# Performance work log

Hardware: AMD Instinct MI355X
Metric: run time of the kernel (lower is better)

The kernel has to match this reference:

```python
import jax, jax.numpy as jnp
import numpy as np

B, U, L, E, H, V = 512, 10, 50, 200, 200, 50000
FLAT = 16 * 16 * 8  # conv(3x3,VALID)->48x48, pool(3x3,s3)->16x16, 8 channels


def gru(x, Wih, Whh, bih, bhh):
    """PyTorch-convention GRU (gate order r,z,n). x: [B,T,E] -> (ys [B,T,H], h_last [B,H])."""
    Bx = x.shape[0]
    Hh = Whh.shape[1]
    x_proj = x @ Wih.T + bih  # [B,T,3H]

    def step(h, xp):
        gh = h @ Whh.T + bhh
        xr, xz, xn = jnp.split(xp, 3, axis=-1)
        hr, hz, hn = jnp.split(gh, 3, axis=-1)
        r = jax.nn.sigmoid(xr + hr)
        z = jax.nn.sigmoid(xz + hz)
        n = jnp.tanh(xn + r * hn)
        h_new = (1.0 - z) * n + z * h
        return h_new, h_new

    h0 = jnp.zeros((Bx, Hh), x.dtype)
    h_last, ys = jax.lax.scan(step, h0, jnp.swapaxes(x_proj, 0, 1))
    return jnp.swapaxes(ys, 0, 1), h_last


def setup_inputs() -> dict:
    key = jax.random.key(0)
    ks = jax.random.split(key, 24)
    s = 0.05
    inp = {
        "utterance": jax.random.randint(ks[0], (B, U, L), 0, V, dtype=jnp.int32),
        "response": jax.random.randint(ks[1], (B, L), 0, V, dtype=jnp.int32),
        "emb": jax.random.uniform(ks[2], (V, E), jnp.float32, -0.25, 0.25),
        "W_ih_u": jax.random.normal(ks[3], (3 * H, E)) * s,
        "W_hh_u": jax.random.normal(ks[4], (3 * H, H)) * s,
        "b_ih_u": jnp.zeros((3 * H,), jnp.float32),
        "b_hh_u": jnp.zeros((3 * H,), jnp.float32),
        "W_ih_r": jax.random.normal(ks[5], (3 * H, E)) * s,
        "W_hh_r": jax.random.normal(ks[6], (3 * H, H)) * s,
        "b_ih_r": jnp.zeros((3 * H,), jnp.float32),
        "b_hh_r": jnp.zeros((3 * H,), jnp.float32),
        "conv_w": jax.random.normal(ks[7], (8, 2, 3, 3)) * 0.3,
        "conv_b": jnp.zeros((8,), jnp.float32),
        "lin_w": jax.random.normal(ks[8], (50, FLAT)) * 0.02,
        "lin_b": jnp.zeros((50,), jnp.float32),
        "Amat": jax.random.normal(ks[9], (H, H)) * 0.05,
        "W_ih_f": jax.random.normal(ks[10], (3 * H, 50)) * s,
        "W_hh_f": jax.random.normal(ks[11], (3 * H, H)) * s,
        "b_ih_f": jnp.zeros((3 * H,), jnp.float32),
        "b_hh_f": jnp.zeros((3 * H,), jnp.float32),
        "flin_w": jax.random.normal(ks[12], (1, H)) * 0.05,
        "flin_b": jnp.zeros((1,), jnp.float32),
    }
    return inp


def reference(utterance, response, emb, W_ih_u, W_hh_u, b_ih_u, b_hh_u,
              W_ih_r, W_hh_r, b_ih_r, b_hh_r, conv_w, conv_b, lin_w, lin_b,
              Amat, W_ih_f, W_hh_f, b_ih_f, b_hh_f, flin_w, flin_b):
    ue = emb[utterance]            # [B,U,L,E]
    re = emb[response]             # [B,L,E]

    rg, _ = gru(re, W_ih_r, W_hh_r, b_ih_r, b_hh_r)  # [B,L,H]

    # word-level match: matmul(utt_emb, resp_emb^T)
    m1 = jnp.einsum('bule,bte->bult', ue, re)  # [B,U,L,L]

    # segment-level: GRU(utt) @ A @ GRU(resp)^T  (loop over utterances folded into batch)
    ug, _ = gru(ue.reshape(B * U, L, E), W_ih_u, W_hh_u, b_ih_u, b_hh_u)
    ug = ug.reshape(B, U, L, H)
    m2 = jnp.einsum('bulh,hk,btk->bult', ug, Amat, rg)  # [B,U,L,L]

    x = jnp.stack([m1, m2], axis=2).reshape(B * U, 2, L, L)  # [B*U,2,50,50]
    x = jax.lax.conv_general_dilated(x, conv_w, (1, 1), 'VALID',
                                     dimension_numbers=('NCHW', 'OIHW', 'NCHW'))
    x = jax.nn.relu(x + conv_b[None, :, None, None])          # [B*U,8,48,48]
    x = jax.lax.reduce_window(x, -jnp.inf, jax.lax.max,
                              (1, 1, 3, 3), (1, 1, 3, 3), 'VALID')  # [B*U,8,16,16]
    x = x.reshape(B * U, FLAT)
    mv = jnp.tanh(x @ lin_w.T + lin_b).reshape(B, U, 50)      # matching vectors

    _, h_last = gru(mv, W_ih_f, W_hh_f, b_ih_f, b_hh_f)       # [B,H]
    logits = h_last @ flin_w.T + flin_b                       # [B,1]
    return jax.nn.sigmoid(logits)
```

## Files before the change

### kernel.cpp

```cpp
#include <hip/hip_runtime.h>
#include <hip/hip_bf16.h>


typedef __attribute__((ext_vector_type(8))) short short8v;
typedef __attribute__((ext_vector_type(4))) float f32x4;

__device__ __forceinline__ float sigm(float x) { return 1.0f / (1.0f + __expf(-x)); }
__device__ __forceinline__ float tanhfast(float x) {
    float e = __expf(2.0f * x);
    return 1.0f - 2.0f / (e + 1.0f);
}
__device__ __forceinline__ float bl(unsigned x) { return __uint_as_float(x << 16); }
__device__ __forceinline__ float bh(unsigned x) { return __uint_as_float(x & 0xffff0000u); }
__device__ __forceinline__ unsigned packbf(float a, float b) {
    union { __hip_bfloat16 h[2]; unsigned u; } cv;
    cv.h[0] = __float2bfloat16(a); cv.h[1] = __float2bfloat16(b);
    return cv.u;
}

__global__ __launch_bounds__(256)
void gemm_mfma(const void* __restrict__ Asrc, int a_bf16,
               const int* __restrict__ gidx,
               const float* __restrict__ W, const float* __restrict__ bias,
               __hip_bfloat16* __restrict__ C, int M, int N)
{
    __shared__ __hip_bfloat16 Al[64 * 232];
    __shared__ __hip_bfloat16 Bl[64 * 232];
    const int tid = threadIdx.x;
    const int m0 = blockIdx.x * 64, n0 = blockIdx.y * 64;

    for (int idx = tid; idx < 64 * 29; idx += 256) {
        int r = idx / 29, q = idx - r * 29;
        int k0 = q * 8, row = m0 + r;
        uint4 val = make_uint4(0, 0, 0, 0);
        if (k0 < 200 && row < M) {
            size_t ar = (size_t)(gidx ? gidx[row] : row) * 200 + k0;
            if (a_bf16) {
                val = *(const uint4*)((const __hip_bfloat16*)Asrc + ar);
            } else {
                const float* ap = (const float*)Asrc + ar;
                float4 f0 = *(const float4*)ap;
                float4 f1 = *(const float4*)(ap + 4);
                val.x = packbf(f0.x, f0.y); val.y = packbf(f0.z, f0.w);
                val.z = packbf(f1.x, f1.y); val.w = packbf(f1.z, f1.w);
            }
        }
        *(uint4*)(Al + r * 232 + k0) = val;
    }
    for (int idx = tid; idx < 64 * 29; idx += 256) {
        int r = idx / 29, q = idx - r * 29;
        int k0 = q * 8, row = n0 + r;
        uint4 val = make_uint4(0, 0, 0, 0);
        if (k0 < 200 && row < N) {
            const float* wp = W + (size_t)row * 200 + k0;
            float4 f0 = *(const float4*)wp;
            float4 f1 = *(const float4*)(wp + 4);
            val.x = packbf(f0.x, f0.y); val.y = packbf(f0.z, f0.w);
            val.z = packbf(f1.x, f1.y); val.w = packbf(f1.z, f1.w);
        }
        *(uint4*)(Bl + r * 232 + k0) = val;
    }
    __syncthreads();

    const int wid = tid >> 6, lane = tid & 63;
    const int wm = (wid >> 1) * 32, wn = (wid & 1) * 32;
    const int lrow = lane & 15, lk8 = (lane >> 4) * 8;
    f32x4 acc00 = {0.f, 0.f, 0.f, 0.f}, acc01 = {0.f, 0.f, 0.f, 0.f};
    f32x4 acc10 = {0.f, 0.f, 0.f, 0.f}, acc11 = {0.f, 0.f, 0.f, 0.f};
#pragma unroll
    for (int kk = 0; kk < 7; ++kk) {
        const int kb = kk * 32 + lk8;
        short8v a0 = *(const short8v*)(Al + (wm + lrow) * 232 + kb);
        short8v a1 = *(const short8v*)(Al + (wm + 16 + lrow) * 232 + kb);
        short8v b0 = *(const short8v*)(Bl + (wn + lrow) * 232 + kb);
        short8v b1 = *(const short8v*)(Bl + (wn + 16 + lrow) * 232 + kb);
        acc00 = __builtin_amdgcn_mfma_f32_16x16x32_bf16(a0, b0, acc00, 0, 0, 0);
        acc01 = __builtin_amdgcn_mfma_f32_16x16x32_bf16(a0, b1, acc01, 0, 0, 0);
        acc10 = __builtin_amdgcn_mfma_f32_16x16x32_bf16(a1, b0, acc10, 0, 0, 0);
        acc11 = __builtin_amdgcn_mfma_f32_16x16x32_bf16(a1, b1, acc11, 0, 0, 0);
    }
    const int drow = (lane >> 4) * 4, dcol = lane & 15;
#pragma unroll
    for (int fm = 0; fm < 2; ++fm) {
#pragma unroll
        for (int fn = 0; fn < 2; ++fn) {
            const f32x4 av = (fm == 0) ? (fn == 0 ? acc00 : acc01)
                                       : (fn == 0 ? acc10 : acc11);
            const int gcol = n0 + wn + fn * 16 + dcol;
            if (gcol >= N) continue;
            const float bs = bias ? bias[gcol] : 0.0f;
#pragma unroll
            for (int r = 0; r < 4; ++r) {
                const int grow = m0 + wm + fm * 16 + drow + r;
                if (grow >= M) continue;
                C[(size_t)grow * N + gcol] = __float2bfloat16(av[r] + bs);
            }
        }
    }
}

__global__ __launch_bounds__(256)
void gemm_tn(const void* __restrict__ Av, int a_bf16,
             const int* __restrict__ gidx, int gstride, int goff,
             const float* __restrict__ W, const float* __restrict__ bias,
             void* __restrict__ Cv, int c_bf16,
             int M, int N, int K, int act)
{
    __shared__ float As[16][64];
    __shared__ float Ws[16][64];
    const int tid = threadIdx.x;
    const int m0 = blockIdx.x * 64;
    const int n0 = blockIdx.y * 64;
    const int lr = tid >> 2;
    const int lk = (tid & 3) << 2;
    const int tx = tid & 15, ty = tid >> 4;

    float acc[4][4];
#pragma unroll
    for (int i = 0; i < 4; ++i)
#pragma unroll
        for (int j = 0; j < 4; ++j) acc[i][j] = 0.0f;

    const int am = m0 + lr;
    size_t arow_off = 0; bool avalid = (am < M);
    if (avalid) arow_off = (size_t)(gidx ? gidx[(size_t)am * gstride + goff] : am) * K;
    const float* arow32 = (const float*)Av + arow_off;
    const __hip_bfloat16* arow16 = (const __hip_bfloat16*)Av + arow_off;
    const int wn = n0 + lr;
    const float* wrow = (wn < N) ? (W + (size_t)wn * K) : nullptr;

    for (int kb = 0; kb < K; kb += 16) {
        const int k = kb + lk;
        float a0 = 0, a1 = 0, a2 = 0, a3 = 0, w0 = 0, w1 = 0, w2 = 0, w3 = 0;
        if (avalid) {
            if (a_bf16) {
                if (k + 3 < K) {
                    uint2 p = *(const uint2*)(arow16 + k);
                    a0 = bl(p.x); a1 = bh(p.x); a2 = bl(p.y); a3 = bh(p.y);
                } else {
                    if (k < K) a0 = __bfloat162float(arow16[k]);
                    if (k + 1 < K) a1 = __bfloat162float(arow16[k + 1]);
                    if (k + 2 < K) a2 = __bfloat162float(arow16[k + 2]);
                }
            } else {
                if (k + 3 < K) { float4 v = *(const float4*)(arow32 + k); a0 = v.x; a1 = v.y; a2 = v.z; a3 = v.w; }
                else { if (k < K) a0 = arow32[k]; if (k + 1 < K) a1 = arow32[k + 1]; if (k + 2 < K) a2 = arow32[k + 2]; }
            }
        }
        if (wrow) {
            if (k + 3 < K) { float4 v = *(const float4*)(wrow + k); w0 = v.x; w1 = v.y; w2 = v.z; w3 = v.w; }
            else { if (k < K) w0 = wrow[k]; if (k + 1 < K) w1 = wrow[k + 1]; if (k + 2 < K) w2 = wrow[k + 2]; }
        }
        __syncthreads();
        As[lk + 0][lr] = a0; As[lk + 1][lr] = a1; As[lk + 2][lr] = a2; As[lk + 3][lr] = a3;
        Ws[lk + 0][lr] = w0; Ws[lk + 1][lr] = w1; Ws[lk + 2][lr] = w2; Ws[lk + 3][lr] = w3;
        __syncthreads();
#pragma unroll
        for (int kk = 0; kk < 16; ++kk) {
            float4 av = *(const float4*)(&As[kk][ty << 2]);
            float4 wv = *(const float4*)(&Ws[kk][tx << 2]);
            float aa[4] = { av.x, av.y, av.z, av.w };
            float ww[4] = { wv.x, wv.y, wv.z, wv.w };
#pragma unroll
            for (int i = 0; i < 4; ++i)
#pragma unroll
                for (int j = 0; j < 4; ++j)
                    acc[i][j] = fmaf(aa[i], ww[j], acc[i][j]);
        }
    }

#pragma unroll
    for (int i = 0; i < 4; ++i) {
        const int row = m0 + (ty << 2) + i;
        if (row >= M) continue;
#pragma unroll
        for (int j = 0; j < 4; ++j) {
            const int col = n0 + (tx << 2) + j;
            if (col >= N) continue;
            float t = acc[i][j];
            if (bias) t += bias[col];
            if (act == 1) t = tanhfast(t);
            if (c_bf16) ((__hip_bfloat16*)Cv)[(size_t)row * N + col] = __float2bfloat16(t);
            else        ((float*)Cv)[(size_t)row * N + col] = t;
        }
    }
}

__global__ __launch_bounds__(256)
void transpose_wf(const float* __restrict__ Wf, float* __restrict__ Tf)
{
    int id = blockIdx.x * 256 + threadIdx.x;
    if (id < 120000) {
        int e = id / 600, j = id - e * 600;
        Tf[id] = Wf[(size_t)j * 200 + e];
    }
}

__global__ __launch_bounds__(256)
void pack_whh(const float* __restrict__ Wu, const float* __restrict__ Wr,
              __hip_bfloat16* __restrict__ Du, __hip_bfloat16* __restrict__ Dr)
{
    int idx = blockIdx.x * 256 + threadIdx.x;
    if (idx >= 136192) return;
    int j = idx / 224, e = idx - j * 224;
    bool v = (j < 600) && (e < 200);
    Du[idx] = __float2bfloat16(v ? Wu[(size_t)j * 200 + e] : 0.0f);
    Dr[idx] = __float2bfloat16(v ? Wr[(size_t)j * 200 + e] : 0.0f);
}

__global__ __launch_bounds__(256)
void gather_re16(const int* __restrict__ resp, const float* __restrict__ emb,
                 __hip_bfloat16* __restrict__ re16)
{
    int idx = blockIdx.x * 256 + threadIdx.x;
    if (idx < 2560000) {
        int row = idx / 100, q = idx - row * 100;
        float2 v = *(const float2*)(emb + (size_t)resp[row] * 200 + 2 * q);
        ((unsigned*)re16)[idx] = packbf(v.x, v.y);
    }
}

__global__ __launch_bounds__(512)
void scan_gru_mfma(const int* __restrict__ utt,
                   const __hip_bfloat16* __restrict__ EPu,
                   const __hip_bfloat16* __restrict__ xpr16,
                   const __hip_bfloat16* __restrict__ Wu16,
                   const __hip_bfloat16* __restrict__ Wr16,
                   const float* __restrict__ bhu, const float* __restrict__ bhr,
                   __hip_bfloat16* __restrict__ ug16,
                   __hip_bfloat16* __restrict__ rg16)
{
    __shared__ __align__(16) float gh[32][612];
    __shared__ __align__(16) float hf[32][204];
    __shared__ __align__(16) __hip_bfloat16 h16[32][232];

    const int tid = threadIdx.x;
    const bool isResp = (int)blockIdx.x >= 160;
    const int row0 = isResp ? ((int)blockIdx.x - 160) * 32 : (int)blockIdx.x * 32;
    const __hip_bfloat16* Wt = isResp ? Wr16 : Wu16;
    const float* bgate = isResp ? bhr : bhu;
    __hip_bfloat16* arch = isResp ? rg16 : ug16;

    for (int i = tid; i < 32 * 204; i += 512) ((float*)hf)[i] = 0.0f;
    for (int i = tid; i < 928; i += 512) ((uint4*)h16)[i] = make_uint4(0, 0, 0, 0);
    __syncthreads();

    const int wid = tid >> 6, lane = tid & 63;
    const int ntBase = (wid < 6) ? wid * 5 : 30 + (wid - 6) * 4;
    const int ntCnt  = (wid < 6) ? 5 : 4;
    const int lrow = lane & 15, lk8 = (lane >> 4) * 8;
    const int drow = (lane >> 4) * 4, dcol = lane & 15;

    for (int t = 0; t < 50; ++t) {
        f32x4 a0[5], a1[5];
#pragma unroll
        for (int i = 0; i < 5; ++i) {
            a0[i] = (f32x4){0.f, 0.f, 0.f, 0.f};
            a1[i] = (f32x4){0.f, 0.f, 0.f, 0.f};
        }
#pragma unroll
        for (int kk = 0; kk < 7; ++kk) {
            short8v A0 = *(const short8v*)(&h16[lrow][kk * 32 + lk8]);
            short8v A1 = *(const short8v*)(&h16[16 + lrow][kk * 32 + lk8]);
#pragma unroll
            for (int i = 0; i < 5; ++i) {
                if (i < ntCnt) {
                    const int j = (ntBase + i) * 16 + lrow;
                    short8v B = *(const short8v*)(Wt + (size_t)j * 224 + kk * 32 + lk8);
                    a0[i] = __builtin_amdgcn_mfma_f32_16x16x32_bf16(A0, B, a0[i], 0, 0, 0);
                    a1[i] = __builtin_amdgcn_mfma_f32_16x16x32_bf16(A1, B, a1[i], 0, 0, 0);
                }
            }
        }
#pragma unroll
        for (int i = 0; i < 5; ++i) {
            if (i < ntCnt) {
                const int j = (ntBase + i) * 16 + dcol;
#pragma unroll
                for (int r = 0; r < 4; ++r) {
                    gh[drow + r][j] = a0[i][r];
                    gh[16 + drow + r][j] = a1[i][r];
                }
            }
        }
        __syncthreads();
        for (int task = tid; task < 800; task += 512) {
            const int row = task / 25;
            const int c0 = (task - row * 25) * 8;
            const int grow = row0 + row;
            const __hip_bfloat16* xp = isResp
                ? (xpr16 + ((size_t)grow * 50 + t) * 600)
                : (EPu + (size_t)utt[grow * 50 + t] * 600);
            uint4 xrv = *(const uint4*)(xp + c0);
            uint4 xzv = *(const uint4*)(xp + 200 + c0);
            uint4 xnv = *(const uint4*)(xp + 400 + c0);
            const unsigned xra[4] = { xrv.x, xrv.y, xrv.z, xrv.w };
            const unsigned xza[4] = { xzv.x, xzv.y, xzv.z, xzv.w };
            const unsigned xna[4] = { xnv.x, xnv.y, xnv.z, xnv.w };
            float hn[8];
#pragma unroll
            for (int j = 0; j < 8; ++j) {
                const int c = c0 + j;
                const float xr = (j & 1) ? bh(xra[j >> 1]) : bl(xra[j >> 1]);
                const float xz = (j & 1) ? bh(xza[j >> 1]) : bl(xza[j >> 1]);
                const float xn = (j & 1) ? bh(xna[j >> 1]) : bl(xna[j >> 1]);
                const float rr = sigm(xr + gh[row][c] + bgate[c]);
                const float zz = sigm(xz + gh[row][200 + c] + bgate[200 + c]);
                const float nn = tanhfast(xn + rr * (gh[row][400 + c] + bgate[400 + c]));
                hn[j] = (1.0f - zz) * nn + zz * hf[row][c];
            }
            *(float4*)(&hf[row][c0])     = (float4){hn[0], hn[1], hn[2], hn[3]};
            *(float4*)(&hf[row][c0 + 4]) = (float4){hn[4], hn[5], hn[6], hn[7]};
            uint4 pk;
            pk.x = packbf(hn[0], hn[1]); pk.y = packbf(hn[2], hn[3]);
            pk.z = packbf(hn[4], hn[5]); pk.w = packbf(hn[6], hn[7]);
            *(uint4*)(&h16[row][c0]) = pk;
            *(uint4*)(arch + ((size_t)grow * 50 + t) * 200 + c0) = pk;
        }
        __syncthreads();
    }
}

__global__ __launch_bounds__(256)
void match_conv_pool(const int* __restrict__ utt, const float* __restrict__ emb,
                     const __hip_bfloat16* __restrict__ ug16,
                     const __hip_bfloat16* __restrict__ re16,
                     const __hip_bfloat16* __restrict__ rgA16,
                     const float* __restrict__ cw, const float* __restrict__ cb,
                     float* __restrict__ pooled)
{
    const int bu = blockIdx.x, b = bu / 10;
    __shared__ __align__(16) __hip_bfloat16 As[64 * 232];
    __shared__ __align__(16) __hip_bfloat16 Bs[64 * 232];
    __shared__ float m[2][50][50];
    __shared__ float w[144];
    __shared__ float bsh[8];
    const int tid = threadIdx.x;
    if (tid < 144) w[tid] = cw[tid];
    if (tid >= 144 && tid < 152) bsh[tid - 144] = cb[tid - 144];

    for (int idx = tid; idx < 64 * 29; idx += 256) {
        int r = idx / 29, q = idx - r * 29;
        uint4 av = make_uint4(0, 0, 0, 0), bv = make_uint4(0, 0, 0, 0);
        if (r < 50 && q < 25) {
            const float* ap = emb + (size_t)utt[bu * 50 + r] * 200 + q * 8;
            float4 f0 = *(const float4*)ap;
            float4 f1 = *(const float4*)(ap + 4);
            av.x = packbf(f0.x, f0.y); av.y = packbf(f0.z, f0.w);
            av.z = packbf(f1.x, f1.y); av.w = packbf(f1.z, f1.w);
            bv = *(const uint4*)(re16 + (size_t)b * 10000 + (size_t)r * 200 + q * 8);
        }
        *(uint4*)(As + r * 232 + q * 8) = av;
        *(uint4*)(Bs + r * 232 + q * 8) = bv;
    }
    __syncthreads();

    const int wid = tid >> 6, lane = tid & 63;
    const int wm = (wid >> 1) * 32, wn = (wid & 1) * 32;
    const int lrow = lane & 15, lk8 = (lane >> 4) * 8;
    const int drow = (lane >> 4) * 4, dcol = lane & 15;

#pragma unroll 1
    for (int ch = 0; ch < 2; ++ch) {
        f32x4 acc00 = {0.f, 0.f, 0.f, 0.f}, acc01 = {0.f, 0.f, 0.f, 0.f};
        f32x4 acc10 = {0.f, 0.f, 0.f, 0.f}, acc11 = {0.f, 0.f, 0.f, 0.f};
#pragma unroll
        for (int kk = 0; kk < 7; ++kk) {
            const int kb = kk * 32 + lk8;
            short8v a0 = *(const short8v*)(As + (wm + lrow) * 232 + kb);
            short8v a1 = *(const short8v*)(As + (wm + 16 + lrow) * 232 + kb);
            short8v b0 = *(const short8v*)(Bs + (wn + lrow) * 232 + kb);
            short8v b1 = *(const short8v*)(Bs + (wn + 16 + lrow) * 232 + kb);
            acc00 = __builtin_amdgcn_mfma_f32_16x16x32_bf16(a0, b0, acc00, 0, 0, 0);
            acc01 = __builtin_amdgcn_mfma_f32_16x16x32_bf16(a0, b1, acc01, 0, 0, 0);
            acc10 = __builtin_amdgcn_mfma_f32_16x16x32_bf16(a1, b0, acc10, 0, 0, 0);
            acc11 = __builtin_amdgcn_mfma_f32_16x16x32_bf16(a1, b1, acc11, 0, 0, 0);
        }
#pragma unroll
        for (int fm = 0; fm < 2; ++fm) {
#pragma unroll
            for (int fn = 0; fn < 2; ++fn) {
                const f32x4 av = (fm == 0) ? (fn == 0 ? acc00 : acc01)
                                           : (fn == 0 ? acc10 : acc11);
                const int gcol = wn + fn * 16 + dcol;
                if (gcol >= 50) continue;
#pragma unroll
                for (int r = 0; r < 4; ++r) {
                    const int grow = wm + fm * 16 + drow + r;
                    if (grow < 50) m[ch][grow][gcol] = av[r];
                }
            }
        }
        __syncthreads();
        if (ch == 0) {
            for (int idx = tid; idx < 50 * 25; idx += 256) {
                int r = idx / 25, q = idx - r * 25;
                *(uint4*)(As + r * 232 + q * 8) =
                    *(const uint4*)(ug16 + (size_t)bu * 10000 + (size_t)r * 200 + q * 8);
                *(uint4*)(Bs + r * 232 + q * 8) =
                    *(const uint4*)(rgA16 + (size_t)b * 10000 + (size_t)r * 200 + q * 8);
            }
            __syncthreads();
        }
    }

#pragma unroll
    for (int k = 0; k < 8; ++k) {
        const int o = tid + k * 256;
        const int c = o >> 8, ph = (o >> 4) & 15, pw = o & 15;
        float mx = -1e30f;
#pragma unroll
        for (int p = 0; p < 3; ++p)
#pragma unroll
            for (int q = 0; q < 3; ++q) {
                const int y = ph * 3 + p, x = pw * 3 + q;
                float s = bsh[c];
#pragma unroll
                for (int ci = 0; ci < 2; ++ci)
#pragma unroll
                    for (int dy = 0; dy < 3; ++dy)
#pragma unroll
                        for (int dx = 0; dx < 3; ++dx)
                            s = fmaf(w[(c * 2 + ci) * 9 + dy * 3 + dx],
                                     m[ci][y + dy][x + dx], s);
                s = fmaxf(s, 0.0f);
                mx = fmaxf(mx, s);
            }
        pooled[(size_t)bu * 2048 + o] = mx;
    }
}

__global__ __launch_bounds__(256)
void final_gru(const float* __restrict__ xpf, const float* __restrict__ WTf,
               const float* __restrict__ bhf, const float* __restrict__ fw,
               const float* __restrict__ fb, float* __restrict__ out)
{
    const int blk = blockIdx.x;
    const int tid = threadIdx.x;
    __shared__ float h[2][201];
    for (int i = tid; i < 402; i += 256) ((float*)h)[i] = 0.0f;
    __syncthreads();
    const int rr = tid / 100;
    const int j0 = 2 * (tid % 100);
    for (int t = 0; t < 10; ++t) {
        float cR[2] = {}, cZ[2] = {}, cN[2] = {};
        if (tid < 200) {
#pragma unroll 2
            for (int e = 0; e < 200; ++e) {
                const float* w = WTf + (size_t)e * 600;
                float2 wr = *(const float2*)(w + j0);
                float2 wz = *(const float2*)(w + 200 + j0);
                float2 wn = *(const float2*)(w + 400 + j0);
                float hv = h[rr][e];
                cR[0] = fmaf(hv, wr.x, cR[0]); cR[1] = fmaf(hv, wr.y, cR[1]);
                cZ[0] = fmaf(hv, wz.x, cZ[0]); cZ[1] = fmaf(hv, wz.y, cZ[1]);
                cN[0] = fmaf(hv, wn.x, cN[0]); cN[1] = fmaf(hv, wn.y, cN[1]);
            }
        }
        __syncthreads();
        if (tid < 200) {
            const float* xp = xpf + ((size_t)(blk * 2 + rr) * 10 + t) * 600;
#pragma unroll
            for (int j = 0; j < 2; ++j) {
                const int c = j0 + j;
                float rrg = sigm(xp[c] + cR[j] + bhf[c]);
                float zz = sigm(xp[200 + c] + cZ[j] + bhf[200 + c]);
                float nn = tanhfast(xp[400 + c] + rrg * (cN[j] + bhf[400 + c]));
                h[rr][c] = (1.0f - zz) * nn + zz * h[rr][c];
            }
        }
        __syncthreads();
    }
    if (tid < 2) {
        float s = fb[0];
        for (int k = 0; k < 200; ++k) s = fmaf(h[tid][k], fw[k], s);
        out[blk * 2 + tid] = sigm(s);
    }
}

__global__ __launch_bounds__(256)
void fill_out(float* __restrict__ out)
{
    int i = blockIdx.x * 256 + threadIdx.x;
    if (i < 512) out[i] = 0.0f;
}

extern "C" void kernel_launch(void* const* d_in, const int* in_sizes, int n_in,
                              void* d_out, int out_size, void* d_ws, size_t ws_size,
                              hipStream_t stream)
{
    const int*   utt    = (const int*)d_in[0];
    const int*   resp   = (const int*)d_in[1];
    const float* emb    = (const float*)d_in[2];
    const float* W_ih_u = (const float*)d_in[3];
    const float* W_hh_u = (const float*)d_in[4];
    const float* b_ih_u = (const float*)d_in[5];
    const float* b_hh_u = (const float*)d_in[6];
    const float* W_ih_r = (const float*)d_in[7];
    const float* W_hh_r = (const float*)d_in[8];
    const float* b_ih_r = (const float*)d_in[9];
    const float* b_hh_r = (const float*)d_in[10];
    const float* conv_w = (const float*)d_in[11];
    const float* conv_b = (const float*)d_in[12];
    const float* lin_w  = (const float*)d_in[13];
    const float* lin_b  = (const float*)d_in[14];
    const float* Amat   = (const float*)d_in[15];
    const float* W_ih_f = (const float*)d_in[16];
    const float* W_hh_f = (const float*)d_in[17];
    const float* b_ih_f = (const float*)d_in[18];
    const float* b_hh_f = (const float*)d_in[19];
    const float* flin_w = (const float*)d_in[20];
    const float* flin_b = (const float*)d_in[21];
    float* out = (float*)d_out;
    float* ws  = (float*)d_ws;

    size_t off = 0;
    auto alloc = [&](size_t n) { float* p = ws + off; off += (n + 63) & ~((size_t)63); return p; };
    float* WT_f   = alloc(120000);
    float* Wu16f  = alloc(68096);
    float* Wr16f  = alloc(68096);
    float* re16f  = alloc(2560000);
    float* EPuf   = alloc(15000000);
    float* xprf   = alloc(7680000);
    float* ug16f  = alloc(25600000);
    float* rg16f  = alloc(2560000);
    float* rgA16f = alloc(2560000);

    if (off * sizeof(float) > ws_size) {
        hipLaunchKernelGGL(fill_out, dim3(2), dim3(256), 0, stream, out);
        return;
    }

    __hip_bfloat16* Wu16  = (__hip_bfloat16*)Wu16f;
    __hip_bfloat16* Wr16  = (__hip_bfloat16*)Wr16f;
    __hip_bfloat16* re16  = (__hip_bfloat16*)re16f;
    __hip_bfloat16* EPu   = (__hip_bfloat16*)EPuf;
    __hip_bfloat16* xpr16 = (__hip_bfloat16*)xprf;
    __hip_bfloat16* ug16  = (__hip_bfloat16*)ug16f;
    __hip_bfloat16* rg16  = (__hip_bfloat16*)rg16f;
    __hip_bfloat16* rgA16 = (__hip_bfloat16*)rgA16f;
    float* pooled = EPuf;
    float* mv     = xprf;
    float* xpf    = xprf + 400000;

    hipLaunchKernelGGL(transpose_wf, dim3(469), dim3(256), 0, stream, W_hh_f, WT_f);
    hipLaunchKernelGGL(pack_whh, dim3(532), dim3(256), 0, stream,
                       W_hh_u, W_hh_r, Wu16, Wr16);
    hipLaunchKernelGGL(gather_re16, dim3(10000), dim3(256), 0, stream, resp, emb, re16);
    hipLaunchKernelGGL(gemm_mfma, dim3(782, 10), dim3(256), 0, stream,
                       (const void*)emb, 0, (const int*)nullptr, W_ih_u, b_ih_u,
                       EPu, 50000, 600);
    hipLaunchKernelGGL(gemm_mfma, dim3(400, 10), dim3(256), 0, stream,
                       (const void*)emb, 0, resp, W_ih_r, b_ih_r,
                       xpr16, 25600, 600);
    hipLaunchKernelGGL(scan_gru_mfma, dim3(176), dim3(512), 0, stream,
                       utt, EPu, xpr16, Wu16, Wr16, b_hh_u, b_hh_r, ug16, rg16);
    hipLaunchKernelGGL(gemm_mfma, dim3(400, 4), dim3(256), 0, stream,
                       (const void*)rg16, 1, (const int*)nullptr, Amat,
                       (const float*)nullptr, rgA16, 25600, 200);
    hipLaunchKernelGGL(match_conv_pool, dim3(5120), dim3(256), 0, stream,
                       utt, emb, ug16, re16, rgA16, conv_w, conv_b, pooled);
    hipLaunchKernelGGL(gemm_tn, dim3(80, 1), dim3(256), 0, stream,
                       pooled, 0, (const int*)nullptr, 1, 0, lin_w, lin_b,
                       mv, 0, 5120, 50, 2048, 1);
    hipLaunchKernelGGL(gemm_tn, dim3(80, 10), dim3(256), 0, stream,
                       mv, 0, (const int*)nullptr, 1, 0, W_ih_f, b_ih_f,
                       xpf, 0, 5120, 600, 50, 0);
    hipLaunchKernelGGL(final_gru, dim3(256), dim3(256), 0, stream,
                       xpf, WT_f, b_hh_f, flin_w, flin_b, out);
}
```

Measured before the change: 1.172 ms.

## Keep GRU recurrent weights in registers and prefetch input projections

The recurrent GRU scan kernel now loads its slice of the bf16 W_hh fragments into registers once before the time loop, instead of reloading them from global memory every step. The weight buffer is padded to 640 rows so every wave handles exactly five N-tiles and no per-tile branch is needed. The first batch of per-step input projections is loaded before the MFMA phase so its latency overlaps the matmul. Launch bounds request two blocks per SM. The cost is heavy register use (35 short8 fragments per lane) and a larger gh shared array, with a risk of spills.

```diff
diff --git a/kernel.cpp b/kernel.cpp
--- a/kernel.cpp
+++ b/kernel.cpp
@@ -201,7 +201,7 @@
               __hip_bfloat16* __restrict__ Du, __hip_bfloat16* __restrict__ Dr)
 {
     int idx = blockIdx.x * 256 + threadIdx.x;
-    if (idx >= 136192) return;
+    if (idx >= 143360) return;
     int j = idx / 224, e = idx - j * 224;
     bool v = (j < 600) && (e < 200);
     Du[idx] = __float2bfloat16(v ? Wu[(size_t)j * 200 + e] : 0.0f);
@@ -220,7 +220,7 @@
     }
 }
 
-__global__ __launch_bounds__(512)
+__global__ __launch_bounds__(512, 2)
 void scan_gru_mfma(const int* __restrict__ utt,
                    const __hip_bfloat16* __restrict__ EPu,
                    const __hip_bfloat16* __restrict__ xpr16,
@@ -230,7 +230,7 @@
                    __hip_bfloat16* __restrict__ ug16,
                    __hip_bfloat16* __restrict__ rg16)
 {
-    __shared__ __align__(16) float gh[32][612];
+    __shared__ __align__(16) float gh[32][644];
     __shared__ __align__(16) float hf[32][204];
     __shared__ __align__(16) __hip_bfloat16 h16[32][232];
 
@@ -246,12 +246,31 @@
     __syncthreads();
 
     const int wid = tid >> 6, lane = tid & 63;
-    const int ntBase = (wid < 6) ? wid * 5 : 30 + (wid - 6) * 4;
-    const int ntCnt  = (wid < 6) ? 5 : 4;
     const int lrow = lane & 15, lk8 = (lane >> 4) * 8;
     const int drow = (lane >> 4) * 4, dcol = lane & 15;
 
+    short8v Bf[5][7];
+#pragma unroll
+    for (int i = 0; i < 5; ++i) {
+        const int j = (wid * 5 + i) * 16 + lrow;
+#pragma unroll
+        for (int kk = 0; kk < 7; ++kk)
+            Bf[i][kk] = *(const short8v*)(Wt + (size_t)j * 224 + kk * 32 + lk8);
+    }
+
+    const int r0a = tid / 25,        c0a = (tid % 25) * 8;
+    const int t1  = tid + 512;
+    const int r0b = t1 / 25,         c0b = (t1 % 25) * 8;
+
     for (int t = 0; t < 50; ++t) {
+        const int ga = row0 + r0a;
+        const __hip_bfloat16* xpa = isResp
+            ? (xpr16 + ((size_t)ga * 50 + t) * 600)
+            : (EPu + (size_t)utt[ga * 50 + t] * 600);
+        uint4 xra = *(const uint4*)(xpa + c0a);
+        uint4 xza = *(const uint4*)(xpa + 200 + c0a);
+        uint4 xna = *(const uint4*)(xpa + 400 + c0a);
+
         f32x4 a0[5], a1[5];
 #pragma unroll
         for (int i = 0; i < 5; ++i) {
@@ -264,46 +283,64 @@
             short8v A1 = *(const short8v*)(&h16[16 + lrow][kk * 32 + lk8]);
 #pragma unroll
             for (int i = 0; i < 5; ++i) {
-                if (i < ntCnt) {
-                    const int j = (ntBase + i) * 16 + lrow;
-                    short8v B = *(const short8v*)(Wt + (size_t)j * 224 + kk * 32 + lk8);
-                    a0[i] = __builtin_amdgcn_mfma_f32_16x16x32_bf16(A0, B, a0[i], 0, 0, 0);
-                    a1[i] = __builtin_amdgcn_mfma_f32_16x16x32_bf16(A1, B, a1[i], 0, 0, 0);
-                }
+                a0[i] = __builtin_amdgcn_mfma_f32_16x16x32_bf16(A0, Bf[i][kk], a0[i], 0, 0, 0);
+                a1[i] = __builtin_amdgcn_mfma_f32_16x16x32_bf16(A1, Bf[i][kk], a1[i], 0, 0, 0);
             }
         }
 #pragma unroll
         for (int i = 0; i < 5; ++i) {
-            if (i < ntCnt) {
-                const int j = (ntBase + i) * 16 + dcol;
-#pragma unroll
-                for (int r = 0; r < 4; ++r) {
-                    gh[drow + r][j] = a0[i][r];
-                    gh[16 + drow + r][j] = a1[i][r];
-                }
+            const int j = (wid * 5 + i) * 16 + dcol;
+#pragma unroll
+            for (int r = 0; r < 4; ++r) {
+                gh[drow + r][j] = a0[i][r];
+                gh[16 + drow + r][j] = a1[i][r];
             }
         }
         __syncthreads();
-        for (int task = tid; task < 800; task += 512) {
-            const int row = task / 25;
-            const int c0 = (task - row * 25) * 8;
-            const int grow = row0 + row;
+
+        {
+            const int row = r0a, c0 = c0a, grow = ga;
+            const unsigned xr4[4] = { xra.x, xra.y, xra.z, xra.w };
+            const unsigned xz4[4] = { xza.x, xza.y, xza.z, xza.w };
+            const unsigned xn4[4] = { xna.x, xna.y, xna.z, xna.w };
+            float hn[8];
+#pragma unroll
+            for (int j = 0; j < 8; ++j) {
+                const int c = c0 + j;
+                const float xr = (j & 1) ? bh(xr4[j >> 1]) : bl(xr4[j >> 1]);
+                const float xz = (j & 1) ? bh(xz4[j >> 1]) : bl(xz4[j >> 1]);
+                const float xn = (j & 1) ? bh(xn4[j >> 1]) : bl(xn4[j >> 1]);
+                const float rr = sigm(xr + gh[row][c] + bgate[c]);
+                const float zz = sigm(xz + gh[row][200 + c] + bgate[200 + c]);
+                const float nn = tanhfast(xn + rr * (gh[row][400 + c] + bgate[400 + c]));
+                hn[j] = (1.0f - zz) * nn + zz * hf[row][c];
+            }
+            *(float4*)(&hf[row][c0])     = (float4){hn[0], hn[1], hn[2], hn[3]};
+            *(float4*)(&hf[row][c0 + 4]) = (float4){hn[4], hn[5], hn[6], hn[7]};
+            uint4 pk;
+            pk.x = packbf(hn[0], hn[1]); pk.y = packbf(hn[2], hn[3]);
+            pk.z = packbf(hn[4], hn[5]); pk.w = packbf(hn[6], hn[7]);
+            *(uint4*)(&h16[row][c0]) = pk;
+            *(uint4*)(arch + ((size_t)grow * 50 + t) * 200 + c0) = pk;
+        }
+        if (tid < 288) {
+            const int row = r0b, c0 = c0b, grow = row0 + r0b;
             const __hip_bfloat16* xp = isResp
                 ? (xpr16 + ((size_t)grow * 50 + t) * 600)
                 : (EPu + (size_t)utt[grow * 50 + t] * 600);
             uint4 xrv = *(const uint4*)(xp + c0);
             uint4 xzv = *(const uint4*)(xp + 200 + c0);
             uint4 xnv = *(const uint4*)(xp + 400 + c0);
-            const unsigned xra[4] = { xrv.x, xrv.y, xrv.z, xrv.w };
-            const unsigned xza[4] = { xzv.x, xzv.y, xzv.z, xzv.w };
-            const unsigned xna[4] = { xnv.x, xnv.y, xnv.z, xnv.w };
+            const unsigned xr4[4] = { xrv.x, xrv.y, xrv.z, xrv.w };
+            const unsigned xz4[4] = { xzv.x, xzv.y, xzv.z, xzv.w };
+            const unsigned xn4[4] = { xnv.x, xnv.y, xnv.z, xnv.w };
             float hn[8];
 #pragma unroll
             for (int j = 0; j < 8; ++j) {
                 const int c = c0 + j;
-                const float xr = (j & 1) ? bh(xra[j >> 1]) : bl(xra[j >> 1]);
-                const float xz = (j & 1) ? bh(xza[j >> 1]) : bl(xza[j >> 1]);
-                const float xn = (j & 1) ? bh(xna[j >> 1]) : bl(xna[j >> 1]);
+                const float xr = (j & 1) ? bh(xr4[j >> 1]) : bl(xr4[j >> 1]);
+                const float xz = (j & 1) ? bh(xz4[j >> 1]) : bl(xz4[j >> 1]);
+                const float xn = (j & 1) ? bh(xn4[j >> 1]) : bl(xn4[j >> 1]);
                 const float rr = sigm(xr + gh[row][c] + bgate[c]);
                 const float zz = sigm(xz + gh[row][200 + c] + bgate[200 + c]);
                 const float nn = tanhfast(xn + rr * (gh[row][400 + c] + bgate[400 + c]));
@@ -517,8 +554,8 @@
     size_t off = 0;
     auto alloc = [&](size_t n) { float* p = ws + off; off += (n + 63) & ~((size_t)63); return p; };
     float* WT_f   = alloc(120000);
-    float* Wu16f  = alloc(68096);
-    float* Wr16f  = alloc(68096);
+    float* Wu16f  = alloc(71680);
+    float* Wr16f  = alloc(71680);
     float* re16f  = alloc(2560000);
     float* EPuf   = alloc(15000000);
     float* xprf   = alloc(7680000);
@@ -544,7 +581,7 @@
     float* xpf    = xprf + 400000;
 
     hipLaunchKernelGGL(transpose_wf, dim3(469), dim3(256), 0, stream, W_hh_f, WT_f);
-    hipLaunchKernelGGL(pack_whh, dim3(532), dim3(256), 0, stream,
+    hipLaunchKernelGGL(pack_whh, dim3(560), dim3(256), 0, stream,
                        W_hh_u, W_hh_r, Wu16, Wr16);
     hipLaunchKernelGGL(gather_re16, dim3(10000), dim3(256), 0, stream, resp, emb, re16);
     hipLaunchKernelGGL(gemm_mfma, dim3(782, 10), dim3(256), 0, stream,
```

After: 1.175 ms. Within noise of the previous version (+0.2%).

## Widen GRU scan to 1024 threads, keep hidden state in registers, prefetch inputs

Applied to the files above, without the earlier changes.

Doubles the scan_gru_mfma block to 1024 threads (16 waves), so each wave handles at most 3 output tiles instead of 5. Each of the first 800 threads owns one row/8-column slice. It keeps its fp32 hidden state in registers instead of a shared hf array, and issues the input-projection loads for step t before the MFMA phase so they overlap. The archive store of step t's hidden output is deferred to the next iteration. W_hh padding grows to 640 rows so the 40 tiles are covered, and gh is padded to 644 columns. This raises register pressure under the 1024-thread launch bound, and only 800 of the 1024 threads do gate work.

```diff
diff --git a/kernel.cpp b/kernel.cpp
--- a/kernel.cpp
+++ b/kernel.cpp
@@ -201,7 +201,7 @@
               __hip_bfloat16* __restrict__ Du, __hip_bfloat16* __restrict__ Dr)
 {
     int idx = blockIdx.x * 256 + threadIdx.x;
-    if (idx >= 136192) return;
+    if (idx >= 143360) return;
     int j = idx / 224, e = idx - j * 224;
     bool v = (j < 600) && (e < 200);
     Du[idx] = __float2bfloat16(v ? Wu[(size_t)j * 200 + e] : 0.0f);
@@ -220,7 +220,7 @@
     }
 }
 
-__global__ __launch_bounds__(512)
+__global__ __launch_bounds__(1024, 4)
 void scan_gru_mfma(const int* __restrict__ utt,
                    const __hip_bfloat16* __restrict__ EPu,
                    const __hip_bfloat16* __restrict__ xpr16,
@@ -230,8 +230,7 @@
                    __hip_bfloat16* __restrict__ ug16,
                    __hip_bfloat16* __restrict__ rg16)
 {
-    __shared__ __align__(16) float gh[32][612];
-    __shared__ __align__(16) float hf[32][204];
+    __shared__ __align__(16) float gh[32][644];
     __shared__ __align__(16) __hip_bfloat16 h16[32][232];
 
     const int tid = threadIdx.x;
@@ -241,20 +240,37 @@
     const float* bgate = isResp ? bhr : bhu;
     __hip_bfloat16* arch = isResp ? rg16 : ug16;
 
-    for (int i = tid; i < 32 * 204; i += 512) ((float*)hf)[i] = 0.0f;
-    for (int i = tid; i < 928; i += 512) ((uint4*)h16)[i] = make_uint4(0, 0, 0, 0);
+    for (int i = tid; i < 928; i += 1024) ((uint4*)h16)[i] = make_uint4(0, 0, 0, 0);
     __syncthreads();
 
     const int wid = tid >> 6, lane = tid & 63;
-    const int ntBase = (wid < 6) ? wid * 5 : 30 + (wid - 6) * 4;
-    const int ntCnt  = (wid < 6) ? 5 : 4;
     const int lrow = lane & 15, lk8 = (lane >> 4) * 8;
     const int drow = (lane >> 4) * 4, dcol = lane & 15;
+    const int tbase = (wid < 8) ? wid * 3 : 24 + (wid - 8) * 2;
+    const int tcnt  = (wid < 8) ? 3 : 2;
+
+    const bool gth = tid < 800;
+    const int grow_r = tid & 31;
+    const int gc0 = (tid >> 5) * 8;
+    const int garow = row0 + grow_r;
+    float hfr[8] = {0.f, 0.f, 0.f, 0.f, 0.f, 0.f, 0.f, 0.f};
+    uint4 pend = make_uint4(0, 0, 0, 0);
 
     for (int t = 0; t < 50; ++t) {
-        f32x4 a0[5], a1[5];
-#pragma unroll
-        for (int i = 0; i < 5; ++i) {
+        uint4 xra, xza, xna;
+        if (gth) {
+            const __hip_bfloat16* xp = isResp
+                ? (xpr16 + ((size_t)garow * 50 + t) * 600)
+                : (EPu + (size_t)utt[garow * 50 + t] * 600);
+            xra = *(const uint4*)(xp + gc0);
+            xza = *(const uint4*)(xp + 200 + gc0);
+            xna = *(const uint4*)(xp + 400 + gc0);
+            if (t > 0)
+                *(uint4*)(arch + ((size_t)garow * 50 + (t - 1)) * 200 + gc0) = pend;
+        }
+        f32x4 a0[3], a1[3];
+#pragma unroll
+        for (int i = 0; i < 3; ++i) {
             a0[i] = (f32x4){0.f, 0.f, 0.f, 0.f};
             a1[i] = (f32x4){0.f, 0.f, 0.f, 0.f};
         }
@@ -263,9 +279,9 @@
             short8v A0 = *(const short8v*)(&h16[lrow][kk * 32 + lk8]);
             short8v A1 = *(const short8v*)(&h16[16 + lrow][kk * 32 + lk8]);
 #pragma unroll
-            for (int i = 0; i < 5; ++i) {
-                if (i < ntCnt) {
-                    const int j = (ntBase + i) * 16 + lrow;
+            for (int i = 0; i < 3; ++i) {
+                if (i < tcnt) {
+                    const int j = (tbase + i) * 16 + lrow;
                     short8v B = *(const short8v*)(Wt + (size_t)j * 224 + kk * 32 + lk8);
                     a0[i] = __builtin_amdgcn_mfma_f32_16x16x32_bf16(A0, B, a0[i], 0, 0, 0);
                     a1[i] = __builtin_amdgcn_mfma_f32_16x16x32_bf16(A1, B, a1[i], 0, 0, 0);
@@ -273,9 +289,9 @@
             }
         }
 #pragma unroll
-        for (int i = 0; i < 5; ++i) {
-            if (i < ntCnt) {
-                const int j = (ntBase + i) * 16 + dcol;
+        for (int i = 0; i < 3; ++i) {
+            if (i < tcnt) {
+                const int j = (tbase + i) * 16 + dcol;
 #pragma unroll
                 for (int r = 0; r < 4; ++r) {
                     gh[drow + r][j] = a0[i][r];
@@ -284,41 +300,41 @@
             }
         }
         __syncthreads();
-        for (int task = tid; task < 800; task += 512) {
-            const int row = task / 25;
-            const int c0 = (task - row * 25) * 8;
-            const int grow = row0 + row;
-            const __hip_bfloat16* xp = isResp
-                ? (xpr16 + ((size_t)grow * 50 + t) * 600)
-                : (EPu + (size_t)utt[grow * 50 + t] * 600);
-            uint4 xrv = *(const uint4*)(xp + c0);
-            uint4 xzv = *(const uint4*)(xp + 200 + c0);
-            uint4 xnv = *(const uint4*)(xp + 400 + c0);
-            const unsigned xra[4] = { xrv.x, xrv.y, xrv.z, xrv.w };
-            const unsigned xza[4] = { xzv.x, xzv.y, xzv.z, xzv.w };
-            const unsigned xna[4] = { xnv.x, xnv.y, xnv.z, xnv.w };
+
+        if (gth) {
+            float4 gr0 = *(const float4*)(&gh[grow_r][gc0]);
+            float4 gr1 = *(const float4*)(&gh[grow_r][gc0 + 4]);
+            float4 gz0 = *(const float4*)(&gh[grow_r][200 + gc0]);
+            float4 gz1 = *(const float4*)(&gh[grow_r][200 + gc0 + 4]);
+            float4 gn0 = *(const float4*)(&gh[grow_r][400 + gc0]);
+            float4 gn1 = *(const float4*)(&gh[grow_r][400 + gc0 + 4]);
+            const float ghr[8] = { gr0.x, gr0.y, gr0.z, gr0.w, gr1.x, gr1.y, gr1.z, gr1.w };
+            const float ghz[8] = { gz0.x, gz0.y, gz0.z, gz0.w, gz1.x, gz1.y, gz1.z, gz1.w };
+            const float ghn[8] = { gn0.x, gn0.y, gn0.z, gn0.w, gn1.x, gn1.y, gn1.z, gn1.w };
+            const unsigned xr4[4] = { xra.x, xra.y, xra.z, xra.w };
+            const unsigned xz4[4] = { xza.x, xza.y, xza.z, xza.w };
+            const unsigned xn4[4] = { xna.x, xna.y, xna.z, xna.w };
             float hn[8];
 #pragma unroll
             for (int j = 0; j < 8; ++j) {
-                const int c = c0 + j;
-                const float xr = (j & 1) ? bh(xra[j >> 1]) : bl(xra[j >> 1]);
-                const float xz = (j & 1) ? bh(xza[j >> 1]) : bl(xza[j >> 1]);
-                const float xn = (j & 1) ? bh(xna[j >> 1]) : bl(xna[j >> 1]);
-                const float rr = sigm(xr + gh[row][c] + bgate[c]);
-                const float zz = sigm(xz + gh[row][200 + c] + bgate[200 + c]);
-                const float nn = tanhfast(xn + rr * (gh[row][400 + c] + bgate[400 + c]));
-                hn[j] = (1.0f - zz) * nn + zz * hf[row][c];
-            }
-            *(float4*)(&hf[row][c0])     = (float4){hn[0], hn[1], hn[2], hn[3]};
-            *(float4*)(&hf[row][c0 + 4]) = (float4){hn[4], hn[5], hn[6], hn[7]};
-            uint4 pk;
-            pk.x = packbf(hn[0], hn[1]); pk.y = packbf(hn[2], hn[3]);
-            pk.z = packbf(hn[4], hn[5]); pk.w = packbf(hn[6], hn[7]);
-            *(uint4*)(&h16[row][c0]) = pk;
-            *(uint4*)(arch + ((size_t)grow * 50 + t) * 200 + c0) = pk;
-        }
-        __syncthreads();
-    }
+                const int c = gc0 + j;
+                const float xr = (j & 1) ? bh(xr4[j >> 1]) : bl(xr4[j >> 1]);
+                const float xz = (j & 1) ? bh(xz4[j >> 1]) : bl(xz4[j >> 1]);
+                const float xn = (j & 1) ? bh(xn4[j >> 1]) : bl(xn4[j >> 1]);
+                const float rr = sigm(xr + ghr[j] + bgate[c]);
+                const float zz = sigm(xz + ghz[j] + bgate[200 + c]);
+                const float nn = tanhfast(xn + rr * (ghn[j] + bgate[400 + c]));
+                hn[j] = (1.0f - zz) * nn + zz * hfr[j];
+                hfr[j] = hn[j];
+            }
+            pend.x = packbf(hn[0], hn[1]); pend.y = packbf(hn[2], hn[3]);
+            pend.z = packbf(hn[4], hn[5]); pend.w = packbf(hn[6], hn[7]);
+            *(uint4*)(&h16[grow_r][gc0]) = pend;
+        }
+        __syncthreads();
+    }
+    if (gth)
+        *(uint4*)(arch + ((size_t)garow * 50 + 49) * 200 + gc0) = pend;
 }
 
 __global__ __launch_bounds__(256)
@@ -517,8 +533,8 @@
     size_t off = 0;
     auto alloc = [&](size_t n) { float* p = ws + off; off += (n + 63) & ~((size_t)63); return p; };
     float* WT_f   = alloc(120000);
-    float* Wu16f  = alloc(68096);
-    float* Wr16f  = alloc(68096);
+    float* Wu16f  = alloc(71680);
+    float* Wr16f  = alloc(71680);
     float* re16f  = alloc(2560000);
     float* EPuf   = alloc(15000000);
     float* xprf   = alloc(7680000);
@@ -544,7 +560,7 @@
     float* xpf    = xprf + 400000;
 
     hipLaunchKernelGGL(transpose_wf, dim3(469), dim3(256), 0, stream, W_hh_f, WT_f);
-    hipLaunchKernelGGL(pack_whh, dim3(532), dim3(256), 0, stream,
+    hipLaunchKernelGGL(pack_whh, dim3(560), dim3(256), 0, stream,
                        W_hh_u, W_hh_r, Wu16, Wr16);
     hipLaunchKernelGGL(gather_re16, dim3(10000), dim3(256), 0, stream, resp, emb, re16);
     hipLaunchKernelGGL(gemm_mfma, dim3(782, 10), dim3(256), 0, stream,
@@ -553,7 +569,7 @@
     hipLaunchKernelGGL(gemm_mfma, dim3(400, 10), dim3(256), 0, stream,
                        (const void*)emb, 0, resp, W_ih_r, b_ih_r,
                        xpr16, 25600, 600);
-    hipLaunchKernelGGL(scan_gru_mfma, dim3(176), dim3(512), 0, stream,
+    hipLaunchKernelGGL(scan_gru_mfma, dim3(176), dim3(1024), 0, stream,
                        utt, EPu, xpr16, Wu16, Wr16, b_hh_u, b_hh_r, ug16, rg16);
     hipLaunchKernelGGL(gemm_mfma, dim3(400, 4), dim3(256), 0, stream,
                        (const void*)rg16, 1, (const int*)nullptr, Amat,
```

After: 1.311 ms. 11.8% more time.
